# Optimization experiments

Measured on AMD Instinct MI355X. Metric: run time of the kernel, lower is better.

Reference implementation:

```python
import jax, jax.numpy as jnp
import numpy as np

B, L, H = 2, 256, 256
EXPAND = 2
I = H * EXPAND        # internal_size = 512
S = I                 # state_size must equal internal_size (see broadcast in selective mechanism)
K = 3                 # d_conv (must be odd so 'same' padding holds)
EPS = 1e-5


def _forward(x, W_in, conv_w, conv_b, W_ssm, b_ssm, W_gate, b_gate, A, D, W_out, z, ln_g, ln_b):
    # in_proj: [B,L,H] @ [2I,H]^T -> [B,L,2I] (no bias)
    xp = jnp.einsum('blh,oh->blo', x, W_in)
    x_q, x_k = xp[..., :I], xp[..., I:]
    # conv1d over time, full channel mixing (I -> I), 'same' padding, with bias
    xk = jnp.transpose(x_k, (0, 2, 1))  # [B,I,L]
    xk = jax.lax.conv_general_dilated(xk, conv_w, (1,), [((K - 1) // 2, (K - 1) // 2)],
                                      dimension_numbers=('NCH', 'OIH', 'NCH'))
    xk = xk + conv_b[None, :, None]
    x_k = jnp.transpose(xk, (0, 2, 1))  # [B,L,I]
    x_q = jax.nn.gelu(x_q, approximate=False)  # torch F.gelu default = exact erf
    xc = x_q + x_k  # x_combined [B,L,I]

    # selective mechanism
    ssm = jnp.einsum('bli,oi->blo', xc, W_ssm) + b_ssm      # [B,L,2S+I]
    gate = jax.nn.sigmoid(jnp.einsum('bli,oi->blo', xc, W_gate) + b_gate)  # [B,L,S+I]
    C_w = ssm[..., S:2 * S]          # [B,L,S]
    D_w = ssm[..., 2 * S:]           # [B,L,I]
    C_weight = gate[..., S:] * C_w   # requires S == I
    D_weight = D_w * D_w

    x_out = xc * D_weight            # [B,L,I]
    u = x_out[..., :S]               # state input [B,L,S]

    # recurrence: h_0 = u_0 (broadcast over I); h_t = h_{t-1} * A + u_t (broadcast over I)
    # (init h = 0 reproduces the i==0 branch: 0*A + u_0)
    def step(h, u_t):
        h = h * A + u_t[:, :, None]  # [B,S,I]
        return h, h

    h0 = jnp.zeros((B, S, I), x_out.dtype)
    _, hs = jax.lax.scan(step, h0, jnp.transpose(u, (1, 0, 2)))  # hs: [L,B,S,I]

    C_applied = jnp.einsum('lbsi,bls->bli', hs, C_weight)  # [B,L,I]
    y = C_applied + x_out * D
    out = jnp.einsum('bli,hi->blh', y, W_out)  # out_proj, no bias

    # LayerNorm over last dim
    mu = jnp.mean(out, axis=-1, keepdims=True)
    var = jnp.mean(jnp.square(out - mu), axis=-1, keepdims=True)
    out = (out - mu) * jax.lax.rsqrt(var + EPS) * ln_g + ln_b

    out = out * z  # z is shape (1,)
    return out + x


def setup_inputs() -> dict:
    key = jax.random.key(0)
    ks = jax.random.split(key, 10)
    n = lambda k, shape, s: jax.random.normal(k, shape, jnp.float32) * s
    return {
        'x': n(ks[0], (B, L, H), 1.0),
        'W_in': n(ks[1], (2 * I, H), 1.0 / np.sqrt(H)),
        'conv_w': n(ks[2], (I, I, K), 1.0 / np.sqrt(I * K)),
        'conv_b': n(ks[3], (I,), 0.02),
        'W_ssm': n(ks[4], (2 * S + I, I), 1.0 / np.sqrt(I)),
        'b_ssm': n(ks[5], (2 * S + I,), 0.02),
        'W_gate': n(ks[6], (S + I, I), 1.0 / np.sqrt(I)),
        'b_gate': n(ks[7], (S + I,), 0.02),
        'A': jax.random.uniform(ks[8], (S, I), jnp.float32, 0.0, 0.95),  # keep recurrence stable
        'D': jnp.ones((I,), jnp.float32),
        'W_out': n(ks[9], (H, I), 1.0 / np.sqrt(I)),
        'z': jnp.ones((1,), jnp.float32),
        'ln_g': jnp.ones((H,), jnp.float32),
        'ln_b': jnp.zeros((H,), jnp.float32),
    }


def reference(x, W_in, conv_w, conv_b, W_ssm, b_ssm, W_gate, b_gate, A, D, W_out, z, ln_g, ln_b):
    return _forward(x, W_in, conv_w, conv_b, W_ssm, b_ssm, W_gate, b_gate, A, D, W_out, z, ln_g, ln_b)
```

## Files before the change

### kernel.cpp

```cpp
#include <hip/hip_runtime.h>
#include <math.h>

#define NB    2
#define LSEQ  256
#define HDIM  256
#define IDIM  512
#define NROW  512
#define NC    8
#define TCH   32

typedef __attribute__((ext_vector_type(8))) short bf16x8;
typedef __attribute__((ext_vector_type(4))) float f32x4;

__device__ inline unsigned short f2b(float f) {
    unsigned u = __float_as_uint(f);
    return (unsigned short)((u + 0x7FFFu + ((u >> 16) & 1u)) >> 16);
}

__global__ __launch_bounds__(256) void kcvt(const float* __restrict__ x,
                                            const float* __restrict__ W_in,
                                            const float* __restrict__ conv_w,
                                            const float* __restrict__ W_ssm,
                                            const float* __restrict__ W_gate,
                                            const float* __restrict__ b_ssm,
                                            const float* __restrict__ b_gate,
                                            const float* __restrict__ W_out,
                                            unsigned short* __restrict__ xb,
                                            unsigned short* __restrict__ Wb,
                                            unsigned short* __restrict__ cwb,
                                            unsigned short* __restrict__ Wsgb,
                                            float* __restrict__ bsg,
                                            unsigned short* __restrict__ W_outb) {
    const int stride = gridDim.x * 256;
    const int t0 = blockIdx.x * 256 + threadIdx.x;
    for (int i = t0; i < 131072; i += stride) xb[i] = f2b(x[i]);
    for (int i = t0; i < 262144; i += stride) Wb[i] = f2b(W_in[i]);
    for (int d = t0; d < 262144; d += stride) {
        const float* s = conv_w + (size_t)d * 3;
        cwb[d]          = f2b(s[0]);
        cwb[262144 + d] = f2b(s[1]);
        cwb[524288 + d] = f2b(s[2]);
    }
    for (int d = t0; d < 786432; d += stride) {
        int j = d >> 9, i = d & 511;
        float v = (j < 1024) ? W_ssm[(size_t)(512 + j) * 512 + i]
                             : W_gate[(size_t)(j - 512) * 512 + i];
        Wsgb[d] = f2b(v);
    }
    for (int j = t0; j < 1536; j += stride)
        bsg[j] = (j < 1024) ? b_ssm[512 + j] : b_gate[j - 512];
    for (int i = t0; i < 131072; i += stride) W_outb[i] = f2b(W_out[i]);
}

__global__ __launch_bounds__(256) void k1_mfma(const unsigned short* __restrict__ xb,
                                               const unsigned short* __restrict__ Wb,
                                               float* __restrict__ xq_g,
                                               unsigned short* __restrict__ xkb) {
    const int t = threadIdx.x;
    const int w = blockIdx.x * 4 + (t >> 6);
    const int lane = t & 63;
    const int mt = w >> 6, nt = w & 63;
    const int r0 = mt * 16, n0 = nt * 16;
    const int fr = lane & 15, fk = (lane >> 4) * 8;
    const unsigned short* ap = xb + (size_t)(r0 + fr) * HDIM + fk;
    const unsigned short* bp = Wb + (size_t)(n0 + fr) * HDIM + fk;
    f32x4 acc = {0.f, 0.f, 0.f, 0.f};
    #pragma unroll
    for (int k0 = 0; k0 < HDIM; k0 += 32) {
        bf16x8 av = *(const bf16x8*)(ap + k0);
        bf16x8 bv = *(const bf16x8*)(bp + k0);
        acc = __builtin_amdgcn_mfma_f32_16x16x32_bf16(av, bv, acc, 0, 0, 0);
    }
    const int orow = (lane >> 4) * 4;
    const int oc = n0 + fr;
    if (oc < IDIM) {
        #pragma unroll
        for (int j = 0; j < 4; ++j) {
            float v = acc[j];
            xq_g[(size_t)(r0 + orow + j) * IDIM + oc] =
                0.5f * v * (1.0f + erff(v * 0.70710678118654752f));
        }
    } else {
        #pragma unroll
        for (int j = 0; j < 4; ++j)
            xkb[(size_t)(r0 + orow + j) * IDIM + (oc - IDIM)] = f2b(acc[j]);
    }
}

__global__ __launch_bounds__(256) void kxc_mfma(const unsigned short* __restrict__ xkb,
                                                const unsigned short* __restrict__ cwb,
                                                const float* __restrict__ xq_g,
                                                const float* __restrict__ conv_b,
                                                float* __restrict__ xc,
                                                unsigned short* __restrict__ xcb) {
    const int t = threadIdx.x;
    const int w = blockIdx.x * 4 + (t >> 6);
    const int lane = t & 63;
    const int mt = w >> 5, nt = w & 31;
    const int r0 = mt * 16, o0 = nt * 16;
    const int fr = lane & 15, fk = (lane >> 4) * 8;
    const int g = r0 + fr;
    const int lo = r0 & ~255, hi = lo + 256;
    const bool okm = (g - 1 >= lo), okp = (g + 1 < hi);
    const unsigned short* am = xkb + (size_t)(g - 1) * IDIM + fk;
    const unsigned short* a0 = xkb + (size_t)g * IDIM + fk;
    const unsigned short* ap = xkb + (size_t)(g + 1) * IDIM + fk;
    const unsigned short* b0 = cwb + (size_t)(o0 + fr) * IDIM + fk;
    const unsigned short* b1 = b0 + 262144;
    const unsigned short* b2 = b0 + 524288;
    const bf16x8 zz = {0, 0, 0, 0, 0, 0, 0, 0};
    f32x4 acc = {0.f, 0.f, 0.f, 0.f};
    #pragma unroll
    for (int k0 = 0; k0 < IDIM; k0 += 32) {
        bf16x8 avm = okm ? *(const bf16x8*)(am + k0) : zz;
        bf16x8 av0 = *(const bf16x8*)(a0 + k0);
        bf16x8 avp = okp ? *(const bf16x8*)(ap + k0) : zz;
        bf16x8 bv0 = *(const bf16x8*)(b0 + k0);
        bf16x8 bv1 = *(const bf16x8*)(b1 + k0);
        bf16x8 bv2 = *(const bf16x8*)(b2 + k0);
        acc = __builtin_amdgcn_mfma_f32_16x16x32_bf16(avm, bv0, acc, 0, 0, 0);
        acc = __builtin_amdgcn_mfma_f32_16x16x32_bf16(av0, bv1, acc, 0, 0, 0);
        acc = __builtin_amdgcn_mfma_f32_16x16x32_bf16(avp, bv2, acc, 0, 0, 0);
    }
    const int orow = (lane >> 4) * 4;
    const int oc = o0 + fr;
    const float cb = conv_b[oc];
    #pragma unroll
    for (int j = 0; j < 4; ++j) {
        int r = r0 + orow + j;
        float v = acc[j] + xq_g[(size_t)r * IDIM + oc] + cb;
        xc[(size_t)r * IDIM + oc] = v;
        xcb[(size_t)r * IDIM + oc] = f2b(v);
    }
}

__global__ __launch_bounds__(256) void k3f_mfma(const unsigned short* __restrict__ xcb,
                                                const unsigned short* __restrict__ Wsgb,
                                                const float* __restrict__ bsg,
                                                const float* __restrict__ xc,
                                                float* __restrict__ Cw,
                                                float* __restrict__ u) {
    const int t = threadIdx.x;
    const int w = blockIdx.x * 4 + (t >> 6);
    const int lane = t & 63;
    const int mt = w >> 5, nt = w & 31;
    const int r0 = mt * 16, s0 = nt * 16;
    const int fr = lane & 15, fk = (lane >> 4) * 8;
    const unsigned short* ap = xcb + (size_t)(r0 + fr) * IDIM + fk;
    const unsigned short* b0 = Wsgb + (size_t)(s0 + fr) * IDIM + fk;
    const unsigned short* b1 = Wsgb + (size_t)(512 + s0 + fr) * IDIM + fk;
    const unsigned short* b2 = Wsgb + (size_t)(1024 + s0 + fr) * IDIM + fk;
    f32x4 ac0 = {0.f, 0.f, 0.f, 0.f};
    f32x4 ac1 = {0.f, 0.f, 0.f, 0.f};
    f32x4 ac2 = {0.f, 0.f, 0.f, 0.f};
    #pragma unroll
    for (int k0 = 0; k0 < IDIM; k0 += 32) {
        bf16x8 av  = *(const bf16x8*)(ap + k0);
        bf16x8 bv0 = *(const bf16x8*)(b0 + k0);
        bf16x8 bv1 = *(const bf16x8*)(b1 + k0);
        bf16x8 bv2 = *(const bf16x8*)(b2 + k0);
        ac0 = __builtin_amdgcn_mfma_f32_16x16x32_bf16(av, bv0, ac0, 0, 0, 0);
        ac1 = __builtin_amdgcn_mfma_f32_16x16x32_bf16(av, bv1, ac1, 0, 0, 0);
        ac2 = __builtin_amdgcn_mfma_f32_16x16x32_bf16(av, bv2, ac2, 0, 0, 0);
    }
    const int orow = (lane >> 4) * 4;
    const int sc = s0 + fr;
    const float bc = bsg[sc], bd = bsg[512 + sc], bg = bsg[1024 + sc];
    #pragma unroll
    for (int j = 0; j < 4; ++j) {
        int r = r0 + orow + j;
        float craw = ac0[j] + bc;
        float dw   = ac1[j] + bd;
        float graw = ac2[j] + bg;
        float gv = 1.0f / (1.0f + expf(-graw));
        float xcv = xc[(size_t)r * IDIM + sc];
        Cw[(size_t)r * IDIM + sc] = gv * craw;
        u[(size_t)r * IDIM + sc]  = xcv * dw * dw;
    }
}

__global__ __launch_bounds__(256) void k4a_pass1(const float* __restrict__ u,
                                                 const float* __restrict__ A,
                                                 float* __restrict__ C_loc) {
    const int wave = (blockIdx.x * 256 + threadIdx.x) >> 6;
    const int lane = threadIdx.x & 63;
    const int ig = wave & 63;
    const int sh = (wave >> 6) & 1;
    const int c  = (wave >> 7) & (NC - 1);
    const int b  = wave >> 10;
    const int i8 = ig * 8;
    const int s4 = sh * 256 + lane * 4;
    float a[4][8], h[4][8];
    #pragma unroll
    for (int k = 0; k < 4; ++k) {
        float4 a0 = *(const float4*)&A[(size_t)(s4 + k) * IDIM + i8];
        float4 a1 = *(const float4*)&A[(size_t)(s4 + k) * IDIM + i8 + 4];
        a[k][0] = a0.x; a[k][1] = a0.y; a[k][2] = a0.z; a[k][3] = a0.w;
        a[k][4] = a1.x; a[k][5] = a1.y; a[k][6] = a1.z; a[k][7] = a1.w;
        #pragma unroll
        for (int ii = 0; ii < 8; ++ii) h[k][ii] = 0.f;
    }
    const float* ub = u + ((size_t)b * LSEQ + c * TCH) * IDIM;
    for (int l = 0; l < TCH; ++l) {
        float4 u4 = *(const float4*)(ub + l * IDIM + s4);
        float uu[4] = {u4.x, u4.y, u4.z, u4.w};
        #pragma unroll
        for (int ii = 0; ii < 8; ++ii)
            #pragma unroll
            for (int k = 0; k < 4; ++k)
                h[k][ii] = h[k][ii] * a[k][ii] + uu[k];
    }
    #pragma unroll
    for (int ii = 0; ii < 8; ++ii) {
        float4 v;
        v.x = h[0][ii]; v.y = h[1][ii]; v.z = h[2][ii]; v.w = h[3][ii];
        *(float4*)&C_loc[(((size_t)b * NC + c) * IDIM + i8 + ii) * IDIM + s4] = v;
    }
}

__global__ __launch_bounds__(256) void k4b_combine(const float* __restrict__ A,
                                                   float* __restrict__ C_loc) {
    int idx = blockIdx.x * 256 + threadIdx.x;
    int s4 = (idx & 127) * 4;
    int i  = (idx >> 7) & 511;
    int b  = idx >> 16;
    float da[4], h4[4] = {0.0f, 0.0f, 0.0f, 0.0f};
    #pragma unroll
    for (int j = 0; j < 4; ++j) {
        float aa = A[(size_t)(s4 + j) * IDIM + i];
        aa = aa * aa; aa = aa * aa; aa = aa * aa;
        aa = aa * aa; aa = aa * aa;
        da[j] = aa;
    }
    for (int c = 0; c < NC; ++c) {
        size_t base = (((size_t)b * NC + c) * IDIM + i) * IDIM + s4;
        float4 cl = *(const float4*)&C_loc[base];
        float4 hv;
        hv.x = h4[0]; hv.y = h4[1]; hv.z = h4[2]; hv.w = h4[3];
        *(float4*)&C_loc[base] = hv;
        h4[0] = h4[0] * da[0] + cl.x;
        h4[1] = h4[1] * da[1] + cl.y;
        h4[2] = h4[2] * da[2] + cl.z;
        h4[3] = h4[3] * da[3] + cl.w;
    }
}

__global__ __launch_bounds__(256) void k4c_pass2(const float* __restrict__ u,
                                                 const float* __restrict__ Cw,
                                                 const float* __restrict__ A,
                                                 const float* __restrict__ H,
                                                 float* __restrict__ patl) {
    const int wave = (blockIdx.x * 256 + threadIdx.x) >> 6;
    const int lane = threadIdx.x & 63;
    const int ig = wave & 63;
    const int sh = (wave >> 6) & 1;
    const int c  = (wave >> 7) & (NC - 1);
    const int b  = wave >> 10;
    const int i8 = ig * 8;
    const int s4 = sh * 256 + lane * 4;
    float a[4][8], h[4][8];
    #pragma unroll
    for (int k = 0; k < 4; ++k) {
        float4 a0 = *(const float4*)&A[(size_t)(s4 + k) * IDIM + i8];
        float4 a1 = *(const float4*)&A[(size_t)(s4 + k) * IDIM + i8 + 4];
        a[k][0] = a0.x; a[k][1] = a0.y; a[k][2] = a0.z; a[k][3] = a0.w;
        a[k][4] = a1.x; a[k][5] = a1.y; a[k][6] = a1.z; a[k][7] = a1.w;
    }
    #pragma unroll
    for (int ii = 0; ii < 8; ++ii) {
        float4 hv = *(const float4*)&H[(((size_t)b * NC + c) * IDIM + i8 + ii) * IDIM + s4];
        h[0][ii] = hv.x; h[1][ii] = hv.y; h[2][ii] = hv.z; h[3][ii] = hv.w;
    }
    const float* ub = u + (size_t)b * LSEQ * IDIM;
    const float* cb = Cw + (size_t)b * LSEQ * IDIM;
    float* prow = patl + ((size_t)(b * 2 + sh) * LSEQ) * IDIM;
    const bool w8 = ((lane & 7) == 0);
    const int iiw = lane >> 3;
    for (int l = c * TCH; l < c * TCH + TCH; ++l) {
        float4 u4 = *(const float4*)(ub + l * IDIM + s4);
        float4 c4 = *(const float4*)(cb + l * IDIM + s4);
        float uu[4] = {u4.x, u4.y, u4.z, u4.w};
        float cc[4] = {c4.x, c4.y, c4.z, c4.w};
        float p[8];
        #pragma unroll
        for (int ii = 0; ii < 8; ++ii) {
            float acc = 0.f;
            #pragma unroll
            for (int k = 0; k < 4; ++k) {
                h[k][ii] = h[k][ii] * a[k][ii] + uu[k];
                acc += cc[k] * h[k][ii];
            }
            p[ii] = acc;
        }
        #pragma unroll
        for (int ii = 0; ii < 8; ++ii) p[ii] += __shfl_xor(p[ii], 8, 64);
        #pragma unroll
        for (int ii = 0; ii < 8; ++ii) p[ii] += __shfl_xor(p[ii], 16, 64);
        #pragma unroll
        for (int ii = 0; ii < 8; ++ii) p[ii] += __shfl_xor(p[ii], 32, 64);
        float q = (lane & 32) ? ((lane & 16) ? ((lane & 8) ? p[7] : p[6])
                                             : ((lane & 8) ? p[5] : p[4]))
                              : ((lane & 16) ? ((lane & 8) ? p[3] : p[2])
                                             : ((lane & 8) ? p[1] : p[0]));
        q += __shfl_xor(q, 1, 64);
        q += __shfl_xor(q, 2, 64);
        q += __shfl_xor(q, 4, 64);
        if (w8) prow[(size_t)l * IDIM + i8 + iiw] = q;
    }
}

__global__ __launch_bounds__(256) void k4d_add(const float* __restrict__ patl,
                                               const float* __restrict__ u,
                                               const float* __restrict__ D,
                                               unsigned short* __restrict__ ybb) {
    const int idx = (blockIdx.x * 256 + threadIdx.x) * 2;
    const int i = idx & 511;
    const int l = (idx >> 9) & 255;
    const int bb = idx >> 17;
    float2 p0 = *(const float2*)&patl[(((size_t)bb * 2 + 0) * LSEQ + l) * IDIM + i];
    float2 p1 = *(const float2*)&patl[(((size_t)bb * 2 + 1) * LSEQ + l) * IDIM + i];
    float2 uv = *(const float2*)&u[((size_t)bb * LSEQ + l) * IDIM + i];
    float2 dv = *(const float2*)&D[i];
    size_t yo = ((size_t)bb * LSEQ + l) * IDIM + i;
    ybb[yo]     = f2b(p0.x + p1.x + uv.x * dv.x);
    ybb[yo + 1] = f2b(p0.y + p1.y + uv.y * dv.y);
}

__global__ __launch_bounds__(256) void k5a_mfma(const unsigned short* __restrict__ ybb,
                                                const unsigned short* __restrict__ W_outb,
                                                float* __restrict__ outlin) {
    const int t = threadIdx.x;
    const int w = blockIdx.x * 4 + (t >> 6);
    const int lane = t & 63;
    const int mt = w >> 4, nt = w & 15;
    const int r0 = mt * 16, h0 = nt * 16;
    const int fr = lane & 15, fk = (lane >> 4) * 8;
    const unsigned short* ap = ybb + (size_t)(r0 + fr) * IDIM + fk;
    const unsigned short* bp = W_outb + (size_t)(h0 + fr) * IDIM + fk;
    f32x4 acc = {0.f, 0.f, 0.f, 0.f};
    #pragma unroll
    for (int k0 = 0; k0 < IDIM; k0 += 32) {
        bf16x8 av = *(const bf16x8*)(ap + k0);
        bf16x8 bv = *(const bf16x8*)(bp + k0);
        acc = __builtin_amdgcn_mfma_f32_16x16x32_bf16(av, bv, acc, 0, 0, 0);
    }
    const int orow = (lane >> 4) * 4;
    const int hc = h0 + fr;
    #pragma unroll
    for (int j = 0; j < 4; ++j)
        outlin[(size_t)(r0 + orow + j) * HDIM + hc] = acc[j];
}

__global__ __launch_bounds__(256) void k5b_ln(const float* __restrict__ outlin,
                                              const float* __restrict__ x,
                                              const float* __restrict__ z,
                                              const float* __restrict__ ln_g,
                                              const float* __restrict__ ln_b,
                                              float* __restrict__ out) {
    const int r = blockIdx.x;
    const int t = threadIdx.x;
    float v = outlin[(size_t)r * HDIM + t];
    float s1 = v, s2 = v * v;
    #pragma unroll
    for (int off = 1; off < 64; off <<= 1) {
        s1 += __shfl_xor(s1, off, 64);
        s2 += __shfl_xor(s2, off, 64);
    }
    __shared__ float r1[4], r2[4];
    const int w = t >> 6, lane = t & 63;
    if (lane == 0) { r1[w] = s1; r2[w] = s2; }
    __syncthreads();
    float t1 = r1[0] + r1[1] + r1[2] + r1[3];
    float t2 = r2[0] + r2[1] + r2[2] + r2[3];
    float mu = t1 * (1.0f / 256.0f);
    float var = t2 * (1.0f / 256.0f) - mu * mu;
    float inv = rsqrtf(var + 1e-5f);
    float o = (v - mu) * inv * ln_g[t] + ln_b[t];
    out[(size_t)r * HDIM + t] = o * z[0] + x[(size_t)r * HDIM + t];
}

extern "C" void kernel_launch(void* const* d_in, const int* in_sizes, int n_in,
                              void* d_out, int out_size, void* d_ws, size_t ws_size,
                              hipStream_t stream) {
    const float* x      = (const float*)d_in[0];
    const float* W_in   = (const float*)d_in[1];
    const float* conv_w = (const float*)d_in[2];
    const float* conv_b = (const float*)d_in[3];
    const float* W_ssm  = (const float*)d_in[4];
    const float* b_ssm  = (const float*)d_in[5];
    const float* W_gate = (const float*)d_in[6];
    const float* b_gate = (const float*)d_in[7];
    const float* A      = (const float*)d_in[8];
    const float* D      = (const float*)d_in[9];
    const float* W_out  = (const float*)d_in[10];
    const float* z      = (const float*)d_in[11];
    const float* ln_g   = (const float*)d_in[12];
    const float* ln_b   = (const float*)d_in[13];
    float* out = (float*)d_out;

    float* ws = (float*)d_ws;
    float*          xq_g   = ws;
    float*          xc     = ws + 262144;
    float*          patl   = ws;
    float*          Cw     = ws + 524288;
    float*          u      = ws + 786432;
    float*          outlin = ws + 1048576;
    float*          bsg    = ws + 1179648;
    unsigned short* xcb    = (unsigned short*)(ws + 1181696);
    unsigned short* xkb    = (unsigned short*)(ws + 1312768);
    unsigned short* Wsgb   = (unsigned short*)(ws + 1443840);
    unsigned short* W_outb = (unsigned short*)(ws + 1837056);
    unsigned short* ybb    = (unsigned short*)(ws + 1902592);
    float*          area   = ws + 2033664;
    unsigned short* xb     = (unsigned short*)area;
    unsigned short* Wb     = (unsigned short*)(area + 65536);
    unsigned short* cwb    = (unsigned short*)(area + 196608);
    float*          C_loc  = area;

    kcvt       <<<512, 256, 0, stream>>>(x, W_in, conv_w, W_ssm, W_gate, b_ssm,
                                         b_gate, W_out, xb, Wb, cwb, Wsgb, bsg, W_outb);
    k1_mfma    <<<512, 256, 0, stream>>>(xb, Wb, xq_g, xkb);
    kxc_mfma   <<<256, 256, 0, stream>>>(xkb, cwb, xq_g, conv_b, xc, xcb);
    k3f_mfma   <<<256, 256, 0, stream>>>(xcb, Wsgb, bsg, xc, Cw, u);
    k4a_pass1  <<<512, 256, 0, stream>>>(u, A, C_loc);
    k4b_combine<<<512, 256, 0, stream>>>(A, C_loc);
    k4c_pass2  <<<512, 256, 0, stream>>>(u, Cw, A, C_loc, patl);
    k4d_add    <<<512, 256, 0, stream>>>(patl, u, D, ybb);
    k5a_mfma   <<<128, 256, 0, stream>>>(ybb, W_outb, outlin);
    k5b_ln     <<<512, 256, 0, stream>>>(outlin, x, z, ln_g, ln_b, out);
}
```

Baseline: 102.4 us.

## Fold conv weights into in_proj, fuse scan combine and out-proj with LayerNorm

Precomputes the product of the conv weights and the x_k half of W_in so that the conv over x_k becomes three small GEMMs on x directly, with the GELU path fused into the same kernel. The chunk-prefix combine kernel is removed and each pass-2 block recomputes its carry-in state from earlier chunks. The D-skip term is written by the selective-mechanism kernel and the scan results are accumulated into y with atomics. Out-projection and LayerNorm are merged into one kernel. Launches and intermediate buffers drop, in exchange for a weight-weight GEMM on every call, redundant prefix recomputation, atomic contention, and an extra bf16 rounding from the folded weights.

```diff
diff --git a/kernel.cpp b/kernel.cpp
--- a/kernel.cpp
+++ b/kernel.cpp
@@ -26,7 +26,8 @@
                                             const float* __restrict__ b_gate,
                                             const float* __restrict__ W_out,
                                             unsigned short* __restrict__ xb,
-                                            unsigned short* __restrict__ Wb,
+                                            unsigned short* __restrict__ Wqb,
+                                            unsigned short* __restrict__ WgT,
                                             unsigned short* __restrict__ cwb,
                                             unsigned short* __restrict__ Wsgb,
                                             float* __restrict__ bsg,
@@ -34,7 +35,11 @@
     const int stride = gridDim.x * 256;
     const int t0 = blockIdx.x * 256 + threadIdx.x;
     for (int i = t0; i < 131072; i += stride) xb[i] = f2b(x[i]);
-    for (int i = t0; i < 262144; i += stride) Wb[i] = f2b(W_in[i]);
+    for (int i = t0; i < 131072; i += stride) Wqb[i] = f2b(W_in[i]);
+    for (int d = t0; d < 131072; d += stride) {
+        int i = d & 511, h = d >> 9;
+        WgT[(size_t)h * 512 + i] = f2b(W_in[(size_t)(512 + i) * 256 + h]);
+    }
     for (int d = t0; d < 262144; d += stride) {
         const float* s = conv_w + (size_t)d * 3;
         cwb[d]          = f2b(s[0]);
@@ -52,47 +57,49 @@
     for (int i = t0; i < 131072; i += stride) W_outb[i] = f2b(W_out[i]);
 }
 
-__global__ __launch_bounds__(256) void k1_mfma(const unsigned short* __restrict__ xb,
-                                               const unsigned short* __restrict__ Wb,
-                                               float* __restrict__ xq_g,
-                                               unsigned short* __restrict__ xkb) {
+__global__ __launch_bounds__(256) void kW_mfma(const unsigned short* __restrict__ cwb,
+                                               const unsigned short* __restrict__ WgT,
+                                               unsigned short* __restrict__ Wcb) {
     const int t = threadIdx.x;
     const int w = blockIdx.x * 4 + (t >> 6);
     const int lane = t & 63;
-    const int mt = w >> 6, nt = w & 63;
-    const int r0 = mt * 16, n0 = nt * 16;
+    const int mt = w >> 4, nt = w & 15;
+    const int o0 = mt * 16, h0 = nt * 16;
     const int fr = lane & 15, fk = (lane >> 4) * 8;
-    const unsigned short* ap = xb + (size_t)(r0 + fr) * HDIM + fk;
-    const unsigned short* bp = Wb + (size_t)(n0 + fr) * HDIM + fk;
-    f32x4 acc = {0.f, 0.f, 0.f, 0.f};
-    #pragma unroll
-    for (int k0 = 0; k0 < HDIM; k0 += 32) {
-        bf16x8 av = *(const bf16x8*)(ap + k0);
+    const unsigned short* a0 = cwb + (size_t)(o0 + fr) * 512 + fk;
+    const unsigned short* a1 = a0 + 262144;
+    const unsigned short* a2 = a0 + 524288;
+    const unsigned short* bp = WgT + (size_t)(h0 + fr) * 512 + fk;
+    f32x4 ac0 = {0.f, 0.f, 0.f, 0.f};
+    f32x4 ac1 = {0.f, 0.f, 0.f, 0.f};
+    f32x4 ac2 = {0.f, 0.f, 0.f, 0.f};
+    #pragma unroll
+    for (int k0 = 0; k0 < 512; k0 += 32) {
         bf16x8 bv = *(const bf16x8*)(bp + k0);
-        acc = __builtin_amdgcn_mfma_f32_16x16x32_bf16(av, bv, acc, 0, 0, 0);
+        bf16x8 v0 = *(const bf16x8*)(a0 + k0);
+        bf16x8 v1 = *(const bf16x8*)(a1 + k0);
+        bf16x8 v2 = *(const bf16x8*)(a2 + k0);
+        ac0 = __builtin_amdgcn_mfma_f32_16x16x32_bf16(v0, bv, ac0, 0, 0, 0);
+        ac1 = __builtin_amdgcn_mfma_f32_16x16x32_bf16(v1, bv, ac1, 0, 0, 0);
+        ac2 = __builtin_amdgcn_mfma_f32_16x16x32_bf16(v2, bv, ac2, 0, 0, 0);
     }
     const int orow = (lane >> 4) * 4;
-    const int oc = n0 + fr;
-    if (oc < IDIM) {
-        #pragma unroll
-        for (int j = 0; j < 4; ++j) {
-            float v = acc[j];
-            xq_g[(size_t)(r0 + orow + j) * IDIM + oc] =
-                0.5f * v * (1.0f + erff(v * 0.70710678118654752f));
-        }
-    } else {
-        #pragma unroll
-        for (int j = 0; j < 4; ++j)
-            xkb[(size_t)(r0 + orow + j) * IDIM + (oc - IDIM)] = f2b(acc[j]);
-    }
-}
-
-__global__ __launch_bounds__(256) void kxc_mfma(const unsigned short* __restrict__ xkb,
-                                                const unsigned short* __restrict__ cwb,
-                                                const float* __restrict__ xq_g,
-                                                const float* __restrict__ conv_b,
-                                                float* __restrict__ xc,
-                                                unsigned short* __restrict__ xcb) {
+    const int hc = h0 + fr;
+    #pragma unroll
+    for (int j = 0; j < 4; ++j) {
+        size_t o = (size_t)(o0 + orow + j) * 256 + hc;
+        Wcb[o]          = f2b(ac0[j]);
+        Wcb[131072 + o] = f2b(ac1[j]);
+        Wcb[262144 + o] = f2b(ac2[j]);
+    }
+}
+
+__global__ __launch_bounds__(256) void kxc2_mfma(const unsigned short* __restrict__ xb,
+                                                 const unsigned short* __restrict__ Wqb,
+                                                 const unsigned short* __restrict__ Wcb,
+                                                 const float* __restrict__ conv_b,
+                                                 float* __restrict__ xc,
+                                                 unsigned short* __restrict__ xcb) {
     const int t = threadIdx.x;
     const int w = blockIdx.x * 4 + (t >> 6);
     const int lane = t & 63;
@@ -102,25 +109,29 @@
     const int g = r0 + fr;
     const int lo = r0 & ~255, hi = lo + 256;
     const bool okm = (g - 1 >= lo), okp = (g + 1 < hi);
-    const unsigned short* am = xkb + (size_t)(g - 1) * IDIM + fk;
-    const unsigned short* a0 = xkb + (size_t)g * IDIM + fk;
-    const unsigned short* ap = xkb + (size_t)(g + 1) * IDIM + fk;
-    const unsigned short* b0 = cwb + (size_t)(o0 + fr) * IDIM + fk;
-    const unsigned short* b1 = b0 + 262144;
-    const unsigned short* b2 = b0 + 524288;
+    const unsigned short* am = xb + (size_t)(g - 1) * 256 + fk;
+    const unsigned short* a0 = xb + (size_t)g * 256 + fk;
+    const unsigned short* ap = xb + (size_t)(g + 1) * 256 + fk;
+    const unsigned short* bq = Wqb + (size_t)(o0 + fr) * 256 + fk;
+    const unsigned short* b0 = Wcb + (size_t)(o0 + fr) * 256 + fk;
+    const unsigned short* b1 = b0 + 131072;
+    const unsigned short* b2 = b0 + 262144;
     const bf16x8 zz = {0, 0, 0, 0, 0, 0, 0, 0};
-    f32x4 acc = {0.f, 0.f, 0.f, 0.f};
-    #pragma unroll
-    for (int k0 = 0; k0 < IDIM; k0 += 32) {
+    f32x4 accq = {0.f, 0.f, 0.f, 0.f};
+    f32x4 accc = {0.f, 0.f, 0.f, 0.f};
+    #pragma unroll
+    for (int k0 = 0; k0 < 256; k0 += 32) {
         bf16x8 avm = okm ? *(const bf16x8*)(am + k0) : zz;
         bf16x8 av0 = *(const bf16x8*)(a0 + k0);
         bf16x8 avp = okp ? *(const bf16x8*)(ap + k0) : zz;
-        bf16x8 bv0 = *(const bf16x8*)(b0 + k0);
-        bf16x8 bv1 = *(const bf16x8*)(b1 + k0);
-        bf16x8 bv2 = *(const bf16x8*)(b2 + k0);
-        acc = __builtin_amdgcn_mfma_f32_16x16x32_bf16(avm, bv0, acc, 0, 0, 0);
-        acc = __builtin_amdgcn_mfma_f32_16x16x32_bf16(av0, bv1, acc, 0, 0, 0);
-        acc = __builtin_amdgcn_mfma_f32_16x16x32_bf16(avp, bv2, acc, 0, 0, 0);
+        bf16x8 bqv = *(const bf16x8*)(bq + k0);
+        bf16x8 b0v = *(const bf16x8*)(b0 + k0);
+        bf16x8 b1v = *(const bf16x8*)(b1 + k0);
+        bf16x8 b2v = *(const bf16x8*)(b2 + k0);
+        accq = __builtin_amdgcn_mfma_f32_16x16x32_bf16(av0, bqv, accq, 0, 0, 0);
+        accc = __builtin_amdgcn_mfma_f32_16x16x32_bf16(avm, b0v, accc, 0, 0, 0);
+        accc = __builtin_amdgcn_mfma_f32_16x16x32_bf16(av0, b1v, accc, 0, 0, 0);
+        accc = __builtin_amdgcn_mfma_f32_16x16x32_bf16(avp, b2v, accc, 0, 0, 0);
     }
     const int orow = (lane >> 4) * 4;
     const int oc = o0 + fr;
@@ -128,7 +139,9 @@
     #pragma unroll
     for (int j = 0; j < 4; ++j) {
         int r = r0 + orow + j;
-        float v = acc[j] + xq_g[(size_t)r * IDIM + oc] + cb;
+        float q = accq[j];
+        float gl = 0.5f * q * (1.0f + erff(q * 0.70710678118654752f));
+        float v = gl + accc[j] + cb;
         xc[(size_t)r * IDIM + oc] = v;
         xcb[(size_t)r * IDIM + oc] = f2b(v);
     }
@@ -138,8 +151,10 @@
                                                 const unsigned short* __restrict__ Wsgb,
                                                 const float* __restrict__ bsg,
                                                 const float* __restrict__ xc,
+                                                const float* __restrict__ D,
                                                 float* __restrict__ Cw,
-                                                float* __restrict__ u) {
+                                                float* __restrict__ u,
+                                                float* __restrict__ y) {
     const int t = threadIdx.x;
     const int w = blockIdx.x * 4 + (t >> 6);
     const int lane = t & 63;
@@ -166,6 +181,7 @@
     const int orow = (lane >> 4) * 4;
     const int sc = s0 + fr;
     const float bc = bsg[sc], bd = bsg[512 + sc], bg = bsg[1024 + sc];
+    const float Dv = D[sc];
     #pragma unroll
     for (int j = 0; j < 4; ++j) {
         int r = r0 + orow + j;
@@ -174,8 +190,10 @@
         float graw = ac2[j] + bg;
         float gv = 1.0f / (1.0f + expf(-graw));
         float xcv = xc[(size_t)r * IDIM + sc];
+        float uv = xcv * dw * dw;
         Cw[(size_t)r * IDIM + sc] = gv * craw;
-        u[(size_t)r * IDIM + sc]  = xcv * dw * dw;
+        u[(size_t)r * IDIM + sc]  = uv;
+        y[(size_t)r * IDIM + sc]  = uv * Dv;
     }
 }
 
@@ -218,38 +236,11 @@
     }
 }
 
-__global__ __launch_bounds__(256) void k4b_combine(const float* __restrict__ A,
-                                                   float* __restrict__ C_loc) {
-    int idx = blockIdx.x * 256 + threadIdx.x;
-    int s4 = (idx & 127) * 4;
-    int i  = (idx >> 7) & 511;
-    int b  = idx >> 16;
-    float da[4], h4[4] = {0.0f, 0.0f, 0.0f, 0.0f};
-    #pragma unroll
-    for (int j = 0; j < 4; ++j) {
-        float aa = A[(size_t)(s4 + j) * IDIM + i];
-        aa = aa * aa; aa = aa * aa; aa = aa * aa;
-        aa = aa * aa; aa = aa * aa;
-        da[j] = aa;
-    }
-    for (int c = 0; c < NC; ++c) {
-        size_t base = (((size_t)b * NC + c) * IDIM + i) * IDIM + s4;
-        float4 cl = *(const float4*)&C_loc[base];
-        float4 hv;
-        hv.x = h4[0]; hv.y = h4[1]; hv.z = h4[2]; hv.w = h4[3];
-        *(float4*)&C_loc[base] = hv;
-        h4[0] = h4[0] * da[0] + cl.x;
-        h4[1] = h4[1] * da[1] + cl.y;
-        h4[2] = h4[2] * da[2] + cl.z;
-        h4[3] = h4[3] * da[3] + cl.w;
-    }
-}
-
-__global__ __launch_bounds__(256) void k4c_pass2(const float* __restrict__ u,
-                                                 const float* __restrict__ Cw,
-                                                 const float* __restrict__ A,
-                                                 const float* __restrict__ H,
-                                                 float* __restrict__ patl) {
+__global__ __launch_bounds__(256) void k4c2_pass2(const float* __restrict__ u,
+                                                  const float* __restrict__ Cw,
+                                                  const float* __restrict__ A,
+                                                  const float* __restrict__ C_loc,
+                                                  float* __restrict__ y) {
     const int wave = (blockIdx.x * 256 + threadIdx.x) >> 6;
     const int lane = threadIdx.x & 63;
     const int ig = wave & 63;
@@ -265,15 +256,34 @@
         float4 a1 = *(const float4*)&A[(size_t)(s4 + k) * IDIM + i8 + 4];
         a[k][0] = a0.x; a[k][1] = a0.y; a[k][2] = a0.z; a[k][3] = a0.w;
         a[k][4] = a1.x; a[k][5] = a1.y; a[k][6] = a1.z; a[k][7] = a1.w;
-    }
-    #pragma unroll
-    for (int ii = 0; ii < 8; ++ii) {
-        float4 hv = *(const float4*)&H[(((size_t)b * NC + c) * IDIM + i8 + ii) * IDIM + s4];
-        h[0][ii] = hv.x; h[1][ii] = hv.y; h[2][ii] = hv.z; h[3][ii] = hv.w;
+        #pragma unroll
+        for (int ii = 0; ii < 8; ++ii) h[k][ii] = 0.f;
+    }
+    if (c > 0) {
+        float da[4][8];
+        #pragma unroll
+        for (int k = 0; k < 4; ++k)
+            #pragma unroll
+            for (int ii = 0; ii < 8; ++ii) {
+                float aa = a[k][ii];
+                aa = aa * aa; aa = aa * aa; aa = aa * aa;
+                aa = aa * aa; aa = aa * aa;
+                da[k][ii] = aa;
+            }
+        for (int cc = 0; cc < c; ++cc) {
+            #pragma unroll
+            for (int ii = 0; ii < 8; ++ii) {
+                float4 cl = *(const float4*)&C_loc[(((size_t)b * NC + cc) * IDIM + i8 + ii) * IDIM + s4];
+                h[0][ii] = h[0][ii] * da[0][ii] + cl.x;
+                h[1][ii] = h[1][ii] * da[1][ii] + cl.y;
+                h[2][ii] = h[2][ii] * da[2][ii] + cl.z;
+                h[3][ii] = h[3][ii] * da[3][ii] + cl.w;
+            }
+        }
     }
     const float* ub = u + (size_t)b * LSEQ * IDIM;
     const float* cb = Cw + (size_t)b * LSEQ * IDIM;
-    float* prow = patl + ((size_t)(b * 2 + sh) * LSEQ) * IDIM;
+    float* yb = y + (size_t)b * LSEQ * IDIM;
     const bool w8 = ((lane & 7) == 0);
     const int iiw = lane >> 3;
     for (int l = c * TCH; l < c * TCH + TCH; ++l) {
@@ -305,78 +315,63 @@
         q += __shfl_xor(q, 1, 64);
         q += __shfl_xor(q, 2, 64);
         q += __shfl_xor(q, 4, 64);
-        if (w8) prow[(size_t)l * IDIM + i8 + iiw] = q;
-    }
-}
-
-__global__ __launch_bounds__(256) void k4d_add(const float* __restrict__ patl,
-                                               const float* __restrict__ u,
-                                               const float* __restrict__ D,
-                                               unsigned short* __restrict__ ybb) {
-    const int idx = (blockIdx.x * 256 + threadIdx.x) * 2;
-    const int i = idx & 511;
-    const int l = (idx >> 9) & 255;
-    const int bb = idx >> 17;
-    float2 p0 = *(const float2*)&patl[(((size_t)bb * 2 + 0) * LSEQ + l) * IDIM + i];
-    float2 p1 = *(const float2*)&patl[(((size_t)bb * 2 + 1) * LSEQ + l) * IDIM + i];
-    float2 uv = *(const float2*)&u[((size_t)bb * LSEQ + l) * IDIM + i];
-    float2 dv = *(const float2*)&D[i];
-    size_t yo = ((size_t)bb * LSEQ + l) * IDIM + i;
-    ybb[yo]     = f2b(p0.x + p1.x + uv.x * dv.x);
-    ybb[yo + 1] = f2b(p0.y + p1.y + uv.y * dv.y);
-}
-
-__global__ __launch_bounds__(256) void k5a_mfma(const unsigned short* __restrict__ ybb,
-                                                const unsigned short* __restrict__ W_outb,
-                                                float* __restrict__ outlin) {
+        if (w8) atomicAdd(&yb[(size_t)l * IDIM + i8 + iiw], q);
+    }
+}
+
+__global__ __launch_bounds__(1024) void k5ab(const float* __restrict__ y,
+                                             const unsigned short* __restrict__ W_outb,
+                                             const float* __restrict__ x,
+                                             const float* __restrict__ z,
+                                             const float* __restrict__ ln_g,
+                                             const float* __restrict__ ln_b,
+                                             float* __restrict__ out) {
+    __shared__ float sm[16][260];
     const int t = threadIdx.x;
-    const int w = blockIdx.x * 4 + (t >> 6);
-    const int lane = t & 63;
-    const int mt = w >> 4, nt = w & 15;
-    const int r0 = mt * 16, h0 = nt * 16;
+    const int w = t >> 6, lane = t & 63;
+    const int r0 = blockIdx.x * 16;
+    const int h0 = w * 16;
     const int fr = lane & 15, fk = (lane >> 4) * 8;
-    const unsigned short* ap = ybb + (size_t)(r0 + fr) * IDIM + fk;
+    const float* apf = y + (size_t)(r0 + fr) * IDIM + fk;
     const unsigned short* bp = W_outb + (size_t)(h0 + fr) * IDIM + fk;
     f32x4 acc = {0.f, 0.f, 0.f, 0.f};
     #pragma unroll
     for (int k0 = 0; k0 < IDIM; k0 += 32) {
-        bf16x8 av = *(const bf16x8*)(ap + k0);
+        float4 f0 = *(const float4*)(apf + k0);
+        float4 f1 = *(const float4*)(apf + k0 + 4);
+        bf16x8 av;
+        av[0] = (short)f2b(f0.x); av[1] = (short)f2b(f0.y);
+        av[2] = (short)f2b(f0.z); av[3] = (short)f2b(f0.w);
+        av[4] = (short)f2b(f1.x); av[5] = (short)f2b(f1.y);
+        av[6] = (short)f2b(f1.z); av[7] = (short)f2b(f1.w);
         bf16x8 bv = *(const bf16x8*)(bp + k0);
         acc = __builtin_amdgcn_mfma_f32_16x16x32_bf16(av, bv, acc, 0, 0, 0);
     }
     const int orow = (lane >> 4) * 4;
-    const int hc = h0 + fr;
-    #pragma unroll
-    for (int j = 0; j < 4; ++j)
-        outlin[(size_t)(r0 + orow + j) * HDIM + hc] = acc[j];
-}
-
-__global__ __launch_bounds__(256) void k5b_ln(const float* __restrict__ outlin,
-                                              const float* __restrict__ x,
-                                              const float* __restrict__ z,
-                                              const float* __restrict__ ln_g,
-                                              const float* __restrict__ ln_b,
-                                              float* __restrict__ out) {
-    const int r = blockIdx.x;
-    const int t = threadIdx.x;
-    float v = outlin[(size_t)r * HDIM + t];
-    float s1 = v, s2 = v * v;
+    #pragma unroll
+    for (int j = 0; j < 4; ++j) sm[orow + j][h0 + fr] = acc[j];
+    __syncthreads();
+    const int gr = r0 + w;
+    float v[4];
+    #pragma unroll
+    for (int k = 0; k < 4; ++k) v[k] = sm[w][lane + 64 * k];
+    float s1 = v[0] + v[1] + v[2] + v[3];
+    float s2 = v[0] * v[0] + v[1] * v[1] + v[2] * v[2] + v[3] * v[3];
     #pragma unroll
     for (int off = 1; off < 64; off <<= 1) {
         s1 += __shfl_xor(s1, off, 64);
         s2 += __shfl_xor(s2, off, 64);
     }
-    __shared__ float r1[4], r2[4];
-    const int w = t >> 6, lane = t & 63;
-    if (lane == 0) { r1[w] = s1; r2[w] = s2; }
-    __syncthreads();
-    float t1 = r1[0] + r1[1] + r1[2] + r1[3];
-    float t2 = r2[0] + r2[1] + r2[2] + r2[3];
-    float mu = t1 * (1.0f / 256.0f);
-    float var = t2 * (1.0f / 256.0f) - mu * mu;
+    float mu = s1 * (1.0f / 256.0f);
+    float var = s2 * (1.0f / 256.0f) - mu * mu;
     float inv = rsqrtf(var + 1e-5f);
-    float o = (v - mu) * inv * ln_g[t] + ln_b[t];
-    out[(size_t)r * HDIM + t] = o * z[0] + x[(size_t)r * HDIM + t];
+    float z0 = z[0];
+    #pragma unroll
+    for (int k = 0; k < 4; ++k) {
+        int col = lane + 64 * k;
+        float o = (v[k] - mu) * inv * ln_g[col] + ln_b[col];
+        out[(size_t)gr * HDIM + col] = o * z0 + x[(size_t)gr * HDIM + col];
+    }
 }
 
 extern "C" void kernel_launch(void* const* d_in, const int* in_sizes, int n_in,
@@ -399,33 +394,29 @@
     float* out = (float*)d_out;
 
     float* ws = (float*)d_ws;
-    float*          xq_g   = ws;
+    float*          y      = ws;
     float*          xc     = ws + 262144;
-    float*          patl   = ws;
     float*          Cw     = ws + 524288;
     float*          u      = ws + 786432;
-    float*          outlin = ws + 1048576;
-    float*          bsg    = ws + 1179648;
-    unsigned short* xcb    = (unsigned short*)(ws + 1181696);
-    unsigned short* xkb    = (unsigned short*)(ws + 1312768);
-    unsigned short* Wsgb   = (unsigned short*)(ws + 1443840);
-    unsigned short* W_outb = (unsigned short*)(ws + 1837056);
-    unsigned short* ybb    = (unsigned short*)(ws + 1902592);
-    float*          area   = ws + 2033664;
+    float*          bsg    = ws + 1048576;
+    unsigned short* Wsgb   = (unsigned short*)(ws + 1050624);
+    unsigned short* W_outb = (unsigned short*)(ws + 1443840);
+    float*          area   = ws + 1509376;
     unsigned short* xb     = (unsigned short*)area;
-    unsigned short* Wb     = (unsigned short*)(area + 65536);
+    unsigned short* Wqb    = (unsigned short*)(area + 65536);
+    unsigned short* WgT    = (unsigned short*)(area + 131072);
     unsigned short* cwb    = (unsigned short*)(area + 196608);
+    unsigned short* Wcb    = (unsigned short*)(area + 589824);
+    unsigned short* xcb    = (unsigned short*)(area + 786432);
     float*          C_loc  = area;
 
-    kcvt       <<<512, 256, 0, stream>>>(x, W_in, conv_w, W_ssm, W_gate, b_ssm,
-                                         b_gate, W_out, xb, Wb, cwb, Wsgb, bsg, W_outb);
-    k1_mfma    <<<512, 256, 0, stream>>>(xb, Wb, xq_g, xkb);
-    kxc_mfma   <<<256, 256, 0, stream>>>(xkb, cwb, xq_g, conv_b, xc, xcb);
-    k3f_mfma   <<<256, 256, 0, stream>>>(xcb, Wsgb, bsg, xc, Cw, u);
-    k4a_pass1  <<<512, 256, 0, stream>>>(u, A, C_loc);
-    k4b_combine<<<512, 256, 0, stream>>>(A, C_loc);
-    k4c_pass2  <<<512, 256, 0, stream>>>(u, Cw, A, C_loc, patl);
-    k4d_add    <<<512, 256, 0, stream>>>(patl, u, D, ybb);
-    k5a_mfma   <<<128, 256, 0, stream>>>(ybb, W_outb, outlin);
-    k5b_ln     <<<512, 256, 0, stream>>>(outlin, x, z, ln_g, ln_b, out);
-}
+    kcvt      <<<512, 256, 0, stream>>>(x, W_in, conv_w, W_ssm, W_gate, b_ssm,
+                                        b_gate, W_out, xb, Wqb, WgT, cwb, Wsgb,
+                                        bsg, W_outb);
+    kW_mfma   <<<128, 256, 0, stream>>>(cwb, WgT, Wcb);
+    kxc2_mfma <<<256, 256, 0, stream>>>(xb, Wqb, Wcb, conv_b, xc, xcb);
+    k3f_mfma  <<<256, 256, 0, stream>>>(xcb, Wsgb, bsg, xc, D, Cw, u, y);
+    k4a_pass1 <<<512, 256, 0, stream>>>(u, A, C_loc);
+    k4c2_pass2<<<512, 256, 0, stream>>>(u, Cw, A, C_loc, y);
+    k5ab      <<<32, 1024, 0, stream>>>(y, W_outb, x, z, ln_g, ln_b, out);
+}
```

Measured after the change: 113.2 us. 10.5% more time.
